# Performance work log

Measured on AMD Instinct MI355X. Metric: run time of the kernel, lower is better.

Reference implementation:

```python
import math
import jax, jax.numpy as jnp
import numpy as np

C = 256          # channels
HID = 64         # max(int(C*0.25),16)
RH = 64          # max(C//4,32) router hidden
N, S, H, W = 8, 64, 16, 16
LOW_FREQ_RATIO = 0.2
ROUTER_TEMP = 1.0
LN_EPS = 1e-5

def gelu(v):
    return jax.nn.gelu(v, approximate=False)

def bn1d(v, s, b):  # folded eval-mode BatchNorm1d: (N,C,S)
    return v * s[None, :, None] + b[None, :, None]

def conv1x1(v, w, b=None):  # v:(N,Cin,S), w:(Cout,Cin)
    o = jnp.einsum('oc,ncs->nos', w, v)
    if b is not None:
        o = o + b[None, :, None]
    return o

def convk(v, w):  # v:(N,Cin,S), w:(Cout,Cin,K), 'same' padding
    k = w.shape[-1]
    return jax.lax.conv_general_dilated(v, w, (1,), [(k // 2, k // 2)],
                                        dimension_numbers=('NCH', 'OIH', 'NCH'))

def setup_inputs():
    key = jax.random.key(0)
    ks = iter(jax.random.split(key, 64))
    def nrm(shape, sc=0.02):
        return jax.random.normal(next(ks), shape, jnp.float32) * sc
    d = {}
    d['x'] = jax.random.normal(next(ks), (N, C, S, H, W), jnp.float32)
    d['ln_g'] = jnp.ones((C,), jnp.float32)
    d['ln_b'] = jnp.zeros((C,), jnp.float32)
    for k in (3, 5, 7):
        d['mb_w%d' % k] = nrm((C, 3 * C, k))
        d['mb_s%d' % k] = 1.0 + nrm((C,))
        d['mb_b%d' % k] = nrm((C,))
    d['mf_w'] = nrm((C, C)); d['mf_s'] = 1.0 + nrm((C,)); d['mf_b'] = nrm((C,))
    d['pg_w1'] = nrm((HID, 3)); d['pg_s1'] = 1.0 + nrm((HID,)); d['pg_b1'] = nrm((HID,))
    d['pg_w2'] = nrm((C, HID)); d['pg_b2'] = nrm((C,))
    d['pp_w'] = nrm((C, C)); d['pp_s'] = 1.0 + nrm((C,)); d['pp_b'] = nrm((C,))
    d['mg_w'] = nrm((C, 2 * C)); d['mg_b'] = nrm((C,))
    d['mo_w1'] = nrm((C, 3 * C)); d['mo_s1'] = 1.0 + nrm((C,)); d['mo_b1'] = nrm((C,))
    d['mo_w2'] = nrm((C, C))
    d['rt_w1'] = nrm((RH, C + 5)); d['rt_b1'] = nrm((RH,))
    d['rt_w2'] = nrm((3, RH)); d['rt_b2'] = nrm((3,))
    d['bp_w1'] = nrm((C, 4 * C)); d['bp_s1'] = 1.0 + nrm((C,)); d['bp_b1'] = nrm((C,))
    d['bp_w2'] = nrm((C, C))
    d['res_scale'] = jnp.full((1, C, 1), 0.05, jnp.float32)
    d['fg_w'] = nrm((C, C)); d['fg_b'] = nrm((C,))
    d['sg_w'] = nrm((C, C)); d['sg_s'] = 1.0 + nrm((C,)); d['sg_b'] = nrm((C,))
    return d

def _forward(x, ln_g, ln_b, mb_w3, mb_s3, mb_b3, mb_w5, mb_s5, mb_b5,
             mb_w7, mb_s7, mb_b7, mf_w, mf_s, mf_b,
             pg_w1, pg_s1, pg_b1, pg_w2, pg_b2, pp_w, pp_s, pp_b,
             mg_w, mg_b, mo_w1, mo_s1, mo_b1, mo_w2,
             rt_w1, rt_b1, rt_w2, rt_b2, bp_w1, bp_s1, bp_b1, bp_w2,
             res_scale, fg_w, fg_b, sg_w, sg_s, sg_b):
    n, c, s = x.shape[:3]
    x32 = x.astype(jnp.float32)
    desc = x32.mean(axis=(-1, -2))                     # (N,C,S)
    t = desc.transpose(0, 2, 1)                        # (N,S,C)
    mu = t.mean(-1, keepdims=True)
    var = t.var(-1, keepdims=True)
    dn = (((t - mu) / jnp.sqrt(var + LN_EPS)) * ln_g + ln_b).transpose(0, 2, 1)  # (N,C,S)

    def tdiff(v, order):
        dd = v[:, :, order:] - v[:, :, :-order]
        return jnp.pad(dd, ((0, 0), (0, 0), (order, 0)))
    diff1 = tdiff(dn, 1)
    diff2 = tdiff(dn, 2)

    # motion branch (multi-kernel conv1d + BN + GELU)
    mi = jnp.concatenate([dn, diff1, diff2], axis=1)   # (N,3C,S)
    motion = 0.0
    for w, bs, bb in ((mb_w3, mb_s3, mb_b3), (mb_w5, mb_s5, mb_b5), (mb_w7, mb_s7, mb_b7)):
        motion = motion + gelu(bn1d(convk(mi, w), bs, bb))
    motion = gelu(bn1d(conv1x1(motion / 3.0, mf_w), mf_s, mf_b))

    # FFT-based cycle / phase estimation
    tokens = dn.transpose(0, 2, 1)                     # (N,S,C)
    freq = jnp.fft.rfft(tokens, axis=1, norm='ortho')  # (N,F,C) complex
    fe = jnp.abs(freq).mean(-1)                        # (N,F)
    Fb = fe.shape[1]
    low = min(max(int(round(Fb * LOW_FREQ_RATIO)), 1), Fb - 1)
    he = fe[:, low:]
    peak_rel = jnp.argmax(he, axis=-1)                 # (N,)
    peak_idx = peak_rel + low
    peak_val = jnp.take_along_axis(he, peak_rel[:, None], axis=1)
    cycle_conf = peak_val / jnp.maximum(he.sum(axis=1, keepdims=True), 1e-6)  # (N,1)
    peak_norm = peak_idx.astype(jnp.float32)[:, None] / float(Fb - 1)
    mean_freq = freq.mean(-1)                          # (N,F) complex
    dom = jnp.take_along_axis(mean_freq, peak_idx[:, None], axis=1)[:, 0]
    dom_phase = jnp.arctan2(dom.imag, dom.real)
    tax = jnp.arange(s, dtype=jnp.float32)
    ang = (2.0 * math.pi / max(s, 1)) * peak_idx.astype(jnp.float32)
    arg = ang[:, None] * tax[None, :] + dom_phase[:, None]
    phase_cos = jnp.cos(arg)[:, None, :]               # (N,1,S)
    phase_sin = jnp.sin(arg)[:, None, :]

    cycle_token = jnp.broadcast_to(cycle_conf[:, :, None], (n, 1, s))
    pf = jnp.concatenate([phase_cos, phase_sin, cycle_token], axis=1)  # (N,3,S)
    pgate = jax.nn.sigmoid(conv1x1(gelu(bn1d(conv1x1(pf, pg_w1), pg_s1, pg_b1)), pg_w2, pg_b2))
    phase = gelu(bn1d(conv1x1(dn * pgate, pp_w), pp_s, pp_b))

    # bidirectional EMA memory via lax.scan
    gate = jax.nn.sigmoid(conv1x1(jnp.concatenate([dn, jnp.abs(diff1)], axis=1), mg_w, mg_b))
    g = gate.transpose(2, 0, 1)                        # (S,N,C)
    dd = dn.transpose(2, 0, 1)
    def step(st, gd):
        gt, dt = gd
        st = gt * st + (1.0 - gt) * dt
        return st, st
    _, fo = jax.lax.scan(step, dd[0], (g[1:], dd[1:]))
    fwd_mem = jnp.concatenate([dd[:1], fo], axis=0).transpose(1, 2, 0)
    _, bo = jax.lax.scan(step, dd[-1], (g[-2::-1], dd[-2::-1]))
    bwd_mem = jnp.concatenate([dd[-1:], bo], axis=0)[::-1].transpose(1, 2, 0)
    memory = conv1x1(gelu(bn1d(conv1x1(
        jnp.concatenate([dn, fwd_mem, bwd_mem], axis=1), mo_w1), mo_s1, mo_b1)), mo_w2)

    # router
    seq_std = dn.std(axis=2).mean(axis=1, keepdims=True)
    diff_energy = jnp.abs(diff1).mean(axis=(1, 2))[:, None]
    motion_energy = jnp.abs(motion).mean(axis=(1, 2))[:, None]
    memory_energy = jnp.abs(memory - dn).mean(axis=(1, 2))[:, None]
    stats = jnp.concatenate([seq_std, diff_energy, cycle_conf, peak_norm,
                             memory_energy + motion_energy], axis=-1)
    ri = jnp.concatenate([dn.mean(-1), stats], axis=-1)  # (N,C+5)
    hdn = gelu(ri @ rt_w1.T + rt_b1)
    logits = hdn @ rt_w2.T + rt_b2
    bw = jax.nn.softmax(logits / max(ROUTER_TEMP, 1e-6), axis=-1)  # (N,3)
    fused = (bw[:, 0, None, None] * motion + bw[:, 1, None, None] * phase
             + bw[:, 2, None, None] * memory)

    delta = conv1x1(gelu(bn1d(conv1x1(
        jnp.concatenate([dn, fused, motion - phase, memory - dn], axis=1),
        bp_w1), bp_s1, bp_b1)), bp_w2)
    delta = delta * jax.nn.sigmoid(conv1x1(dn, fg_w, fg_b))
    delta = res_scale * delta
    delta = delta[:, :, :, None, None]                 # (N,C,S,1,1)

    sp = x32.mean(axis=2)                              # (N,C,H,W)
    sg_lin = jnp.einsum('oc,nchw->nohw', sg_w, sp)
    sgate = jax.nn.sigmoid(sg_lin * sg_s[None, :, None, None] + sg_b[None, :, None, None])
    delta = delta * sgate[:, :, None, :, :]            # (N,C,S,H,W)
    return x + delta.astype(x.dtype)

def reference(x, ln_g, ln_b, mb_w3, mb_s3, mb_b3, mb_w5, mb_s5, mb_b5,
              mb_w7, mb_s7, mb_b7, mf_w, mf_s, mf_b,
              pg_w1, pg_s1, pg_b1, pg_w2, pg_b2, pp_w, pp_s, pp_b,
              mg_w, mg_b, mo_w1, mo_s1, mo_b1, mo_w2,
              rt_w1, rt_b1, rt_w2, rt_b2, bp_w1, bp_s1, bp_b1, bp_w2,
              res_scale, fg_w, fg_b, sg_w, sg_s, sg_b):
    return _forward(x, ln_g, ln_b, mb_w3, mb_s3, mb_b3, mb_w5, mb_s5, mb_b5,
                    mb_w7, mb_s7, mb_b7, mf_w, mf_s, mf_b,
                    pg_w1, pg_s1, pg_b1, pg_w2, pg_b2, pp_w, pp_s, pp_b,
                    mg_w, mg_b, mo_w1, mo_s1, mo_b1, mo_w2,
                    rt_w1, rt_b1, rt_w2, rt_b2, bp_w1, bp_s1, bp_b1, bp_w2,
                    res_scale, fg_w, fg_b, sg_w, sg_s, sg_b)
```

## Files before the change

### kernel.cpp

```cpp
#include <hip/hip_runtime.h>
#include <math.h>

namespace {

constexpr int N_ = 8, C_ = 256, S_ = 64, HW_ = 256;
constexpr int NS = N_ * S_;
constexpr int NHW = N_ * HW_;

constexpr size_t O_DESC  = 0;
constexpr size_t O_DN    = 131072;
constexpr size_t O_MOT   = 393216;
constexpr size_t O_GATE  = 524288;
constexpr size_t O_MEM   = 786432;
constexpr size_t O_PHASE = 1048576;
constexpr size_t O_DELTA = 1441792;
constexpr size_t O_SCN   = 1572864;
constexpr size_t O_SPT   = 2752512;
constexpr size_t O_SGATE = 3276800;
constexpr size_t O_FE    = 3801088;
constexpr size_t O_MFRE  = 3801600;
constexpr size_t O_MFIM  = 3802112;
constexpr size_t O_BW    = 3802656;
constexpr size_t O_ATMF  = 3802688;
constexpr size_t O_ATMG  = 3868224;
constexpr size_t O_ATMO1 = 3999296;
constexpr size_t O_ATMO2 = 4195904;
constexpr size_t O_ATPP  = 4261440;
constexpr size_t O_ATBP1 = 4326976;
constexpr size_t O_ATBP2 = 4589120;
constexpr size_t O_ATFG  = 4654656;
constexpr size_t O_ATSG  = 4720192;
constexpr size_t O_WFRAG = 4785728;
constexpr size_t O_IM2   = 6850112;
constexpr size_t O_CONVC = 8226368;

typedef __attribute__((ext_vector_type(4))) float f32x4;
typedef __attribute__((ext_vector_type(8))) short s16x8;
typedef __attribute__((ext_vector_type(8))) unsigned short u16x8;

__device__ __forceinline__ float gelu_f(float v) {
  return 0.5f * v * (1.0f + erff(v * 0.70710678118654752f));
}
__device__ __forceinline__ float sigmoid_f(float v) {
  return 1.0f / (1.0f + expf(-v));
}
__device__ __forceinline__ unsigned short f2bf(float f) {
  unsigned int u = __float_as_uint(f);
  u += 0x7fffu + ((u >> 16) & 1u);
  return (unsigned short)(u >> 16);
}

__device__ __forceinline__ float block_sum256(float v, float* scratch) {
  #pragma unroll
  for (int off = 32; off; off >>= 1) v += __shfl_down(v, off, 64);
  int w = threadIdx.x >> 6;
  __syncthreads();
  if ((threadIdx.x & 63) == 0) scratch[w] = v;
  __syncthreads();
  return scratch[0] + scratch[1] + scratch[2] + scratch[3];
}

__device__ __forceinline__ void compute_pk(
    int n, const float* __restrict__ fe, const float* __restrict__ mfre,
    const float* __restrict__ mfim,
    float& conf, float& pnorm, float& dph, float& ang) {
  const float* f = fe + n * 33;
  float best = f[7]; int bidx = 0; float hs = 0.f;
  #pragma unroll
  for (int i = 0; i < 26; ++i) {
    float v = f[7 + i];
    hs += v;
    if (v > best) { best = v; bidx = i; }
  }
  int pi = bidx + 7;
  conf = best / fmaxf(hs, 1e-6f);
  pnorm = (float)pi * (1.f / 32.f);
  dph = atan2f(mfim[n * 33 + pi], mfre[n * 33 + pi]);
  ang = (6.283185307179586f / 64.f) * (float)pi;
}

__global__ __launch_bounds__(256) void weights_kernel(
    const float* __restrict__ wmf, const float* __restrict__ wmg,
    const float* __restrict__ wmo1, const float* __restrict__ wmo2,
    const float* __restrict__ wpp, const float* __restrict__ wbp1,
    const float* __restrict__ wbp2, const float* __restrict__ wfg,
    const float* __restrict__ wsg, float* __restrict__ ws,
    const float* __restrict__ w3, const float* __restrict__ w5,
    const float* __restrict__ w7, unsigned short* __restrict__ wf) {
  int bid = blockIdx.x;
  if (bid < 960) {
    __shared__ float tile[32][33];
    int xt = bid % 120, yt = bid / 120;
    const float* src; float* dst; int K;
    if      (xt < 8)   { src = wmf;  dst = ws + O_ATMF;  K = 256;  }
    else if (xt < 24)  { src = wmg;  dst = ws + O_ATMG;  K = 512;  xt -= 8;  }
    else if (xt < 48)  { src = wmo1; dst = ws + O_ATMO1; K = 768;  xt -= 24; }
    else if (xt < 56)  { src = wmo2; dst = ws + O_ATMO2; K = 256;  xt -= 48; }
    else if (xt < 64)  { src = wpp;  dst = ws + O_ATPP;  K = 256;  xt -= 56; }
    else if (xt < 96)  { src = wbp1; dst = ws + O_ATBP1; K = 1024; xt -= 64; }
    else if (xt < 104) { src = wbp2; dst = ws + O_ATBP2; K = 256;  xt -= 96; }
    else if (xt < 112) { src = wfg;  dst = ws + O_ATFG;  K = 256;  xt -= 104;}
    else               { src = wsg;  dst = ws + O_ATSG;  K = 256;  xt -= 112;}
    int tx = threadIdx.x & 31, ty = threadIdx.x >> 5;
    int c = xt * 32 + tx;
    #pragma unroll
    for (int i = 0; i < 4; ++i) {
      int r = yt * 32 + ty + i * 8;
      tile[ty + i * 8][tx] = src[(size_t)r * K + c];
    }
    __syncthreads();
    #pragma unroll
    for (int i = 0; i < 4; ++i) {
      int cc = xt * 32 + ty + i * 8;
      dst[(size_t)cc * 256 + yt * 32 + tx] = tile[tx][ty + i * 8];
    }
  } else {
    int g = (bid - 960) * 256 + threadIdx.x;
    int lane = g & 63;
    int m16 = (g >> 6) % 48;
    int kchunk = (g >> 6) / 48;
    int o = m16 * 16 + (lane & 15);
    int conv = o >> 8, oc = o & 255;
    int q = lane >> 4;
    u16x8 outv;
    #pragma unroll
    for (int j = 0; j < 8; ++j) {
      int k = kchunk * 32 + q * 8 + j;
      int ic = k / 7;
      int tau = k - ic * 7 - 3;
      float v = 0.f;
      if (conv == 0) {
        if (tau >= -1 && tau <= 1) v = w3[((size_t)oc * 768 + ic) * 3 + (tau + 1)];
      } else if (conv == 1) {
        if (tau >= -2 && tau <= 2) v = w5[((size_t)oc * 768 + ic) * 5 + (tau + 2)];
      } else {
        v = w7[((size_t)oc * 768 + ic) * 7 + (tau + 3)];
      }
      outv[j] = f2bf(v);
    }
    *((u16x8*)wf + g) = outv;
  }
}

__global__ __launch_bounds__(256) void reduce_x_kernel(
    const float* __restrict__ x, float* __restrict__ desc_t, float* __restrict__ sp_t) {
  int nc = blockIdx.x; int n = nc >> 8; int c = nc & 255;
  int t = threadIdx.x; int w = t >> 6; int l = t & 63;
  const float4* x4 = (const float4*)x + (size_t)nc * 4096;
  float4 sa = {0.f, 0.f, 0.f, 0.f};
  for (int i = 0; i < 16; ++i) {
    int s = w * 16 + i;
    float4 v = x4[(size_t)s * 64 + l];
    sa.x += v.x; sa.y += v.y; sa.z += v.z; sa.w += v.w;
    float ds = v.x + v.y + v.z + v.w;
    #pragma unroll
    for (int off = 32; off; off >>= 1) ds += __shfl_down(ds, off, 64);
    if (l == 0) desc_t[((size_t)n * 64 + s) * 256 + c] = ds * (1.f / 256.f);
  }
  __shared__ float4 lsp[4][64];
  lsp[w][l] = sa;
  __syncthreads();
  if (t < 64) {
    float4 a = lsp[0][t], b = lsp[1][t], c2 = lsp[2][t], d = lsp[3][t];
    float4 tot;
    tot.x = a.x + b.x + c2.x + d.x; tot.y = a.y + b.y + c2.y + d.y;
    tot.z = a.z + b.z + c2.z + d.z; tot.w = a.w + b.w + c2.w + d.w;
    size_t base = ((size_t)n * 256 + t * 4) * 256 + c;
    sp_t[base]       = tot.x * (1.f / 64.f);
    sp_t[base + 256] = tot.y * (1.f / 64.f);
    sp_t[base + 512] = tot.z * (1.f / 64.f);
    sp_t[base + 768] = tot.w * (1.f / 64.f);
  }
}

__global__ __launch_bounds__(256) void ln_kernel(
    const float* __restrict__ desc_t, const float* __restrict__ g,
    const float* __restrict__ b, float* __restrict__ dn_t) {
  __shared__ float sc[4];
  int col = blockIdx.x; int t = threadIdx.x;
  float v = desc_t[(size_t)col * 256 + t];
  float s1 = block_sum256(v, sc);
  float s2 = block_sum256(v * v, sc);
  float mu = s1 * (1.f / 256.f);
  float var = s2 * (1.f / 256.f) - mu * mu;
  float r = rsqrtf(var + 1e-5f);
  dn_t[(size_t)col * 256 + t] = (v - mu) * r * g[t] + b[t];
}

__global__ __launch_bounds__(256) void gate_kernel(
    const float* __restrict__ dn_t, const float* __restrict__ At_mg,
    const float* __restrict__ mg_b, float* __restrict__ gate_t) {
  __shared__ float gin[512];
  int col = blockIdx.x; int t = threadIdx.x; int s = col & 63;
  float d = dn_t[(size_t)col * 256 + t];
  float d1 = (s >= 1) ? d - dn_t[(size_t)(col - 1) * 256 + t] : 0.f;
  gin[t] = d;
  gin[256 + t] = fabsf(d1);
  __syncthreads();
  float a0 = 0.f, a1 = 0.f, a2 = 0.f, a3 = 0.f;
  #pragma unroll 4
  for (int k = 0; k < 512; k += 4) {
    a0 += At_mg[(size_t)(k + 0) * 256 + t] * gin[k + 0];
    a1 += At_mg[(size_t)(k + 1) * 256 + t] * gin[k + 1];
    a2 += At_mg[(size_t)(k + 2) * 256 + t] * gin[k + 2];
    a3 += At_mg[(size_t)(k + 3) * 256 + t] * gin[k + 3];
  }
  gate_t[(size_t)col * 256 + t] = sigmoid_f(((a0 + a1) + (a2 + a3)) + mg_b[t]);
}

__global__ __launch_bounds__(256) void dnaux_kernel(
    const float* __restrict__ dn_t, unsigned short* __restrict__ imf,
    float* __restrict__ fe, float* __restrict__ mfre, float* __restrict__ mfim) {
  int bid = blockIdx.x;
  int t = threadIdx.x;
  if (bid < 1344) {
    int g = bid * 256 + t;
    int lane = g & 63;
    int c16 = (g >> 6) % 32;
    int kchunk = (g >> 6) / 32;
    int col = c16 * 16 + (lane & 15);
    int n = col >> 6, s = col & 63;
    int q = lane >> 4;
    const float* base = dn_t + (size_t)n * 16384;
    u16x8 outv;
    #pragma unroll
    for (int j = 0; j < 8; ++j) {
      int k = kchunk * 32 + q * 8 + j;
      int ic = k / 7;
      int tau = k - ic * 7 - 3;
      int stream = ic >> 8, c = ic & 255;
      int sp = s + tau;
      float v = 0.f;
      if (sp >= 0 && sp < 64) {
        float d = base[(size_t)sp * 256 + c];
        if (stream == 0) v = d;
        else if (stream == 1) v = (sp >= 1) ? d - base[(size_t)(sp - 1) * 256 + c] : 0.f;
        else v = (sp >= 2) ? d - base[(size_t)(sp - 2) * 256 + c] : 0.f;
      }
      outv[j] = f2bf(v);
    }
    *((u16x8*)imf + g) = outv;
  } else {
    int b = bid - 1344; int n = b / 33; int f = b % 33;
    __shared__ float cs[64], sn[64];
    __shared__ float sc[4];
    if (t < 64) {
      int ft = (f * t) & 63;
      float ang = -6.283185307179586f * (float)ft * (1.f / 64.f);
      cs[t] = cosf(ang); sn[t] = sinf(ang);
    }
    __syncthreads();
    float re = 0.f, im = 0.f;
    const float* base = dn_t + (size_t)n * 16384 + t;
    for (int s = 0; s < 64; ++s) {
      float v = base[(size_t)s * 256];
      re += v * cs[s]; im += v * sn[s];
    }
    re *= 0.125f; im *= 0.125f;
    float mag = sqrtf(re * re + im * im);
    float sm = block_sum256(mag, sc);
    float sr = block_sum256(re, sc);
    float si = block_sum256(im, sc);
    if (t == 0) {
      fe[b]   = sm * (1.f / 256.f);
      mfre[b] = sr * (1.f / 256.f);
      mfim[b] = si * (1.f / 256.f);
    }
  }
}

__global__ __launch_bounds__(256) void conv_mfma_kernel(
    const unsigned short* __restrict__ wf, const unsigned short* __restrict__ imf,
    float* __restrict__ partial) {
  int mt = blockIdx.x, nt = blockIdx.y, kp = blockIdx.z;
  int lane = threadIdx.x & 63;
  int w = threadIdx.x >> 6;
  int m16 = mt * 4 + w;
  const s16x8* wfp = (const s16x8*)wf;
  const s16x8* imp = (const s16x8*)imf;
  f32x4 acc0 = {0.f,0.f,0.f,0.f}, acc1 = {0.f,0.f,0.f,0.f};
  f32x4 acc2 = {0.f,0.f,0.f,0.f}, acc3 = {0.f,0.f,0.f,0.f};
  #pragma unroll 2
  for (int cc = 0; cc < 42; ++cc) {
    int kc = kp * 42 + cc;
    s16x8 a = wfp[(size_t)(kc * 48 + m16) * 64 + lane];
    s16x8 b0 = imp[(size_t)(kc * 32 + nt * 4 + 0) * 64 + lane];
    s16x8 b1 = imp[(size_t)(kc * 32 + nt * 4 + 1) * 64 + lane];
    s16x8 b2 = imp[(size_t)(kc * 32 + nt * 4 + 2) * 64 + lane];
    s16x8 b3 = imp[(size_t)(kc * 32 + nt * 4 + 3) * 64 + lane];
    acc0 = __builtin_amdgcn_mfma_f32_16x16x32_bf16(a, b0, acc0, 0, 0, 0);
    acc1 = __builtin_amdgcn_mfma_f32_16x16x32_bf16(a, b1, acc1, 0, 0, 0);
    acc2 = __builtin_amdgcn_mfma_f32_16x16x32_bf16(a, b2, acc2, 0, 0, 0);
    acc3 = __builtin_amdgcn_mfma_f32_16x16x32_bf16(a, b3, acc3, 0, 0, 0);
  }
  int q = lane >> 4, ln = lane & 15;
  int o0 = m16 * 16 + q * 4;
  float* pb = partial + (size_t)kp * 393216;
  #pragma unroll
  for (int r = 0; r < 4; ++r) {
    size_t row = (size_t)(o0 + r) * 512;
    pb[row + (nt * 4 + 0) * 16 + ln] = acc0[r];
    pb[row + (nt * 4 + 1) * 16 + ln] = acc1[r];
    pb[row + (nt * 4 + 2) * 16 + ln] = acc2[r];
    pb[row + (nt * 4 + 3) * 16 + ln] = acc3[r];
  }
}

__global__ __launch_bounds__(256) void motion_kernel(
    const float* __restrict__ P,
    const float* __restrict__ s3, const float* __restrict__ b3,
    const float* __restrict__ s5, const float* __restrict__ b5,
    const float* __restrict__ s7, const float* __restrict__ b7,
    const float* __restrict__ At_mf, const float* __restrict__ mf_s,
    const float* __restrict__ mf_b, float* __restrict__ motion_t) {
  __shared__ float ms[256];
  int col = blockIdx.x; int t = threadIdx.x;
  float v3 = 0.f, v5 = 0.f, v7 = 0.f;
  #pragma unroll
  for (int kp = 0; kp < 4; ++kp) {
    size_t base = (size_t)kp * 393216 + col;
    v3 += P[base + (size_t)t * 512];
    v5 += P[base + (size_t)(t + 256) * 512];
    v7 += P[base + (size_t)(t + 512) * 512];
  }
  float tot = gelu_f(v3 * s3[t] + b3[t]) + gelu_f(v5 * s5[t] + b5[t]) + gelu_f(v7 * s7[t] + b7[t]);
  ms[t] = tot * (1.f / 3.f);
  __syncthreads();
  float a0 = 0.f, a1 = 0.f, a2 = 0.f, a3 = 0.f;
  #pragma unroll 4
  for (int k = 0; k < 256; k += 4) {
    a0 += At_mf[(size_t)(k + 0) * 256 + t] * ms[k + 0];
    a1 += At_mf[(size_t)(k + 1) * 256 + t] * ms[k + 1];
    a2 += At_mf[(size_t)(k + 2) * 256 + t] * ms[k + 2];
    a3 += At_mf[(size_t)(k + 3) * 256 + t] * ms[k + 3];
  }
  motion_t[(size_t)col * 256 + t] = gelu_f(((a0 + a1) + (a2 + a3)) * mf_s[t] + mf_b[t]);
}

__global__ __launch_bounds__(256) void scan_kernel(
    const float* __restrict__ dn_t, const float* __restrict__ gate_t, float* __restrict__ scn) {
  int n = blockIdx.x, half = blockIdx.y;
  int t = threadIdx.x;
  __shared__ float ld[64 * 128];
  __shared__ float lg[64 * 128];
  const float* dsrc = dn_t + (size_t)n * 16384 + half * 128;
  const float* gsrc = gate_t + (size_t)n * 16384 + half * 128;
  for (int i = t; i < 8192; i += 256) {
    int s = i >> 7, j = i & 127;
    ld[i] = dsrc[(size_t)s * 256 + j];
    lg[i] = gsrc[(size_t)s * 256 + j];
  }
  __syncthreads();
  int cl = t & 127;
  int c = half * 128 + cl;
  size_t ob = (size_t)n * 64 * 512 + c;
  if (t < 128) {
    float st = ld[cl];
    scn[ob] = st;
    for (int s = 1; s < 64; ++s) {
      float g = lg[s * 128 + cl], d = ld[s * 128 + cl];
      st = g * st + (1.f - g) * d;
      scn[ob + (size_t)s * 512] = st;
    }
  } else {
    float st = ld[63 * 128 + cl];
    scn[ob + (size_t)63 * 512 + 256] = st;
    for (int s = 62; s >= 0; --s) {
      float g = lg[s * 128 + cl], d = ld[s * 128 + cl];
      st = g * st + (1.f - g) * d;
      scn[ob + (size_t)s * 512 + 256] = st;
    }
  }
}

__global__ __launch_bounds__(256) void memory_kernel(
    const float* __restrict__ dn_t, const float* __restrict__ scn,
    const float* __restrict__ At1, const float* __restrict__ sc1, const float* __restrict__ bi1,
    const float* __restrict__ At2, float* __restrict__ mem_t) {
  __shared__ float bv[768];
  __shared__ float h[256];
  int col = blockIdx.x; int t = threadIdx.x;
  bv[t]       = dn_t[(size_t)col * 256 + t];
  bv[256 + t] = scn[(size_t)col * 512 + t];
  bv[512 + t] = scn[(size_t)col * 512 + 256 + t];
  __syncthreads();
  float a0 = 0.f, a1 = 0.f, a2 = 0.f, a3 = 0.f;
  #pragma unroll 4
  for (int k = 0; k < 768; k += 4) {
    a0 += At1[(size_t)(k + 0) * 256 + t] * bv[k + 0];
    a1 += At1[(size_t)(k + 1) * 256 + t] * bv[k + 1];
    a2 += At1[(size_t)(k + 2) * 256 + t] * bv[k + 2];
    a3 += At1[(size_t)(k + 3) * 256 + t] * bv[k + 3];
  }
  h[t] = gelu_f(((a0 + a1) + (a2 + a3)) * sc1[t] + bi1[t]);
  __syncthreads();
  float c0 = 0.f, c1 = 0.f, c2 = 0.f, c3 = 0.f;
  #pragma unroll 4
  for (int k = 0; k < 256; k += 4) {
    c0 += At2[(size_t)(k + 0) * 256 + t] * h[k + 0];
    c1 += At2[(size_t)(k + 1) * 256 + t] * h[k + 1];
    c2 += At2[(size_t)(k + 2) * 256 + t] * h[k + 2];
    c3 += At2[(size_t)(k + 3) * 256 + t] * h[k + 3];
  }
  mem_t[(size_t)col * 256 + t] = (c0 + c1) + (c2 + c3);
}

__global__ __launch_bounds__(256) void phase_kernel(
    const float* __restrict__ dn_t, const float* __restrict__ fe,
    const float* __restrict__ mfre, const float* __restrict__ mfim,
    const float* __restrict__ pg_w1, const float* __restrict__ pg_s1, const float* __restrict__ pg_b1,
    const float* __restrict__ pg_w2, const float* __restrict__ pg_b2,
    const float* __restrict__ At_pp, const float* __restrict__ pp_s, const float* __restrict__ pp_b,
    float* __restrict__ phase_t) {
  __shared__ float hh[64];
  __shared__ float pin[256];
  int col = blockIdx.x; int n = col >> 6; int s = col & 63; int t = threadIdx.x;
  float conf, pnorm, dph, ang;
  compute_pk(n, fe, mfre, mfim, conf, pnorm, dph, ang);
  (void)pnorm;
  float arg = ang * (float)s + dph;
  float pc = cosf(arg), ps = sinf(arg);
  if (t < 64) {
    float v = pg_w1[t * 3 + 0] * pc + pg_w1[t * 3 + 1] * ps + pg_w1[t * 3 + 2] * conf;
    hh[t] = gelu_f(v * pg_s1[t] + pg_b1[t]);
  }
  __syncthreads();
  float acc = pg_b2[t];
  const float* wrow = pg_w2 + t * 64;
  #pragma unroll 8
  for (int j = 0; j < 64; ++j) acc += wrow[j] * hh[j];
  pin[t] = dn_t[(size_t)col * 256 + t] * sigmoid_f(acc);
  __syncthreads();
  float a0 = 0.f, a1 = 0.f, a2 = 0.f, a3 = 0.f;
  #pragma unroll 4
  for (int k = 0; k < 256; k += 4) {
    a0 += At_pp[(size_t)(k + 0) * 256 + t] * pin[k + 0];
    a1 += At_pp[(size_t)(k + 1) * 256 + t] * pin[k + 1];
    a2 += At_pp[(size_t)(k + 2) * 256 + t] * pin[k + 2];
    a3 += At_pp[(size_t)(k + 3) * 256 + t] * pin[k + 3];
  }
  phase_t[(size_t)col * 256 + t] = gelu_f(((a0 + a1) + (a2 + a3)) * pp_s[t] + pp_b[t]);
}

__global__ __launch_bounds__(256) void router_kernel(
    const float* __restrict__ dn_t, const float* __restrict__ motion_t,
    const float* __restrict__ memory_t,
    const float* __restrict__ fe, const float* __restrict__ mfre,
    const float* __restrict__ mfim,
    const float* __restrict__ rt_w1, const float* __restrict__ rt_b1,
    const float* __restrict__ rt_w2, const float* __restrict__ rt_b2,
    float* __restrict__ bw) {
  int n = blockIdx.x; int c = threadIdx.x;
  __shared__ float ri[261];
  __shared__ float h2[64];
  __shared__ float lg[3];
  __shared__ float sc[4];
  float sum = 0.f, sq = 0.f, ad1 = 0.f, amot = 0.f, amem = 0.f, prev = 0.f;
  for (int s = 0; s < 64; ++s) {
    size_t i = ((size_t)n * 64 + s) * 256 + c;
    float d = dn_t[i];
    sum += d; sq += d * d;
    if (s > 0) ad1 += fabsf(d - prev);
    prev = d;
    amot += fabsf(motion_t[i]);
    amem += fabsf(memory_t[i] - d);
  }
  float mean = sum * (1.f / 64.f);
  float var = sq * (1.f / 64.f) - mean * mean;
  float stdc = sqrtf(fmaxf(var, 0.f));
  ri[c] = mean;
  float rstd = block_sum256(stdc, sc);
  float rad1 = block_sum256(ad1, sc);
  float rmot = block_sum256(amot, sc);
  float rmem = block_sum256(amem, sc);
  if (c == 0) {
    float conf, pnorm, dph, ang;
    compute_pk(n, fe, mfre, mfim, conf, pnorm, dph, ang);
    (void)dph; (void)ang;
    ri[256] = rstd * (1.f / 256.f);
    ri[257] = rad1 * (1.f / 16384.f);
    ri[258] = conf;
    ri[259] = pnorm;
    ri[260] = (rmem + rmot) * (1.f / 16384.f);
  }
  __syncthreads();
  if (c < 64) {
    float acc = rt_b1[c];
    const float* wrow = rt_w1 + c * 261;
    for (int i = 0; i < 261; ++i) acc += wrow[i] * ri[i];
    h2[c] = gelu_f(acc);
  }
  __syncthreads();
  if (c < 3) {
    float acc = rt_b2[c];
    const float* wrow = rt_w2 + c * 64;
    #pragma unroll 8
    for (int j = 0; j < 64; ++j) acc += wrow[j] * h2[j];
    lg[c] = acc;
  }
  __syncthreads();
  if (c == 0) {
    float m = fmaxf(lg[0], fmaxf(lg[1], lg[2]));
    float e0 = expf(lg[0] - m), e1 = expf(lg[1] - m), e2 = expf(lg[2] - m);
    float inv = 1.f / (e0 + e1 + e2);
    bw[n * 3 + 0] = e0 * inv; bw[n * 3 + 1] = e1 * inv; bw[n * 3 + 2] = e2 * inv;
  }
}

__global__ __launch_bounds__(256) void delta_kernel(
    const float* __restrict__ dn_t, const float* __restrict__ motion_t,
    const float* __restrict__ phase_t, const float* __restrict__ mem_t,
    const float* __restrict__ bw,
    const float* __restrict__ At_fg, const float* __restrict__ fg_b,
    const float* __restrict__ At1, const float* __restrict__ sc1, const float* __restrict__ bi1,
    const float* __restrict__ At2, const float* __restrict__ rs,
    float* __restrict__ delta_t) {
  __shared__ float bv[1024];
  __shared__ float h[256];
  int col = blockIdx.x; int n = col >> 6; int t = threadIdx.x;
  size_t i = (size_t)col * 256 + t;
  float d = dn_t[i], m = motion_t[i], p = phase_t[i], me = mem_t[i];
  float w0 = bw[n * 3 + 0], w1 = bw[n * 3 + 1], w2 = bw[n * 3 + 2];
  bv[t]       = d;
  bv[256 + t] = w0 * m + w1 * p + w2 * me;
  bv[512 + t] = m - p;
  bv[768 + t] = me - d;
  __syncthreads();
  float f0 = 0.f, f1 = 0.f, f2 = 0.f, f3 = 0.f;
  #pragma unroll 4
  for (int k = 0; k < 256; k += 4) {
    f0 += At_fg[(size_t)(k + 0) * 256 + t] * bv[k + 0];
    f1 += At_fg[(size_t)(k + 1) * 256 + t] * bv[k + 1];
    f2 += At_fg[(size_t)(k + 2) * 256 + t] * bv[k + 2];
    f3 += At_fg[(size_t)(k + 3) * 256 + t] * bv[k + 3];
  }
  float fgv = sigmoid_f(((f0 + f1) + (f2 + f3)) + fg_b[t]);
  float a0 = 0.f, a1 = 0.f, a2 = 0.f, a3 = 0.f;
  #pragma unroll 4
  for (int k = 0; k < 1024; k += 4) {
    a0 += At1[(size_t)(k + 0) * 256 + t] * bv[k + 0];
    a1 += At1[(size_t)(k + 1) * 256 + t] * bv[k + 1];
    a2 += At1[(size_t)(k + 2) * 256 + t] * bv[k + 2];
    a3 += At1[(size_t)(k + 3) * 256 + t] * bv[k + 3];
  }
  h[t] = gelu_f(((a0 + a1) + (a2 + a3)) * sc1[t] + bi1[t]);
  __syncthreads();
  float c0 = 0.f, c1 = 0.f, c2 = 0.f, c3 = 0.f;
  #pragma unroll 4
  for (int k = 0; k < 256; k += 4) {
    c0 += At2[(size_t)(k + 0) * 256 + t] * h[k + 0];
    c1 += At2[(size_t)(k + 1) * 256 + t] * h[k + 1];
    c2 += At2[(size_t)(k + 2) * 256 + t] * h[k + 2];
    c3 += At2[(size_t)(k + 3) * 256 + t] * h[k + 3];
  }
  delta_t[i] = ((c0 + c1) + (c2 + c3)) * fgv * rs[t];
}

template <int K, int EPI>
__global__ __launch_bounds__(256) void gemm_kernel(
    const float* __restrict__ At, const float* __restrict__ B, float* __restrict__ out,
    const float* __restrict__ sc, const float* __restrict__ bi,
    const float* __restrict__ fg, const float* __restrict__ rs) {
  int t = threadIdx.x;
  int o = blockIdx.x * 64 + (t & 63);
  int col = blockIdx.y * 4 + (t >> 6);
  const float* bp = B + (size_t)col * K;
  float4 a0 = {0.f,0.f,0.f,0.f};
  for (int kk = 0; kk < K; kk += 4) {
    float4 b0 = *(const float4*)(bp + kk);
    a0.x += At[(size_t)(kk + 0) * 256 + o] * b0.x;
    a0.y += At[(size_t)(kk + 1) * 256 + o] * b0.y;
    a0.z += At[(size_t)(kk + 2) * 256 + o] * b0.z;
    a0.w += At[(size_t)(kk + 3) * 256 + o] * b0.w;
  }
  float v0 = (a0.x + a0.y) + (a0.z + a0.w);
  if constexpr (EPI == 4) { v0 = sigmoid_f(v0 * sc[o] + bi[o]); }
  out[(size_t)col * 256 + o] = v0;
}

__global__ __launch_bounds__(256) void final_kernel(
    const float* __restrict__ x, const float* __restrict__ delta_t,
    const float* __restrict__ sgate_t, float* __restrict__ out) {
  int nc = blockIdx.x; int n = nc >> 8; int c = nc & 255;
  int t = threadIdx.x;
  __shared__ float dlt[64];
  __shared__ float4 sgs4[64];
  if (t < 64) dlt[t] = delta_t[((size_t)n * 64 + t) * 256 + c];
  ((float*)sgs4)[t] = sgate_t[((size_t)n * 256 + t) * 256 + c];
  __syncthreads();
  const float4* x4 = (const float4*)x + (size_t)nc * 4096;
  float4* o4 = (float4*)out + (size_t)nc * 4096;
  int w = t >> 6, l = t & 63;
  float4 sg = sgs4[l];
  for (int i = 0; i < 16; ++i) {
    int s = w * 16 + i;
    float d = dlt[s];
    float4 v = x4[(size_t)s * 64 + l];
    v.x += d * sg.x; v.y += d * sg.y; v.z += d * sg.z; v.w += d * sg.w;
    o4[(size_t)s * 64 + l] = v;
  }
}

}

extern "C" void kernel_launch(void* const* d_in, const int* in_sizes, int n_in,
                              void* d_out, int out_size, void* d_ws, size_t ws_size,
                              hipStream_t stream) {
  const float* x      = (const float*)d_in[0];
  const float* ln_g   = (const float*)d_in[1];
  const float* ln_b   = (const float*)d_in[2];
  const float* mb_w3  = (const float*)d_in[3];
  const float* mb_s3  = (const float*)d_in[4];
  const float* mb_b3  = (const float*)d_in[5];
  const float* mb_w5  = (const float*)d_in[6];
  const float* mb_s5  = (const float*)d_in[7];
  const float* mb_b5  = (const float*)d_in[8];
  const float* mb_w7  = (const float*)d_in[9];
  const float* mb_s7  = (const float*)d_in[10];
  const float* mb_b7  = (const float*)d_in[11];
  const float* mf_w   = (const float*)d_in[12];
  const float* mf_s   = (const float*)d_in[13];
  const float* mf_b   = (const float*)d_in[14];
  const float* pg_w1  = (const float*)d_in[15];
  const float* pg_s1  = (const float*)d_in[16];
  const float* pg_b1  = (const float*)d_in[17];
  const float* pg_w2  = (const float*)d_in[18];
  const float* pg_b2  = (const float*)d_in[19];
  const float* pp_w   = (const float*)d_in[20];
  const float* pp_s   = (const float*)d_in[21];
  const float* pp_b   = (const float*)d_in[22];
  const float* mg_w   = (const float*)d_in[23];
  const float* mg_b   = (const float*)d_in[24];
  const float* mo_w1  = (const float*)d_in[25];
  const float* mo_s1  = (const float*)d_in[26];
  const float* mo_b1  = (const float*)d_in[27];
  const float* mo_w2  = (const float*)d_in[28];
  const float* rt_w1  = (const float*)d_in[29];
  const float* rt_b1  = (const float*)d_in[30];
  const float* rt_w2  = (const float*)d_in[31];
  const float* rt_b2  = (const float*)d_in[32];
  const float* bp_w1  = (const float*)d_in[33];
  const float* bp_s1  = (const float*)d_in[34];
  const float* bp_b1  = (const float*)d_in[35];
  const float* bp_w2  = (const float*)d_in[36];
  const float* res_sc = (const float*)d_in[37];
  const float* fg_w   = (const float*)d_in[38];
  const float* fg_b   = (const float*)d_in[39];
  const float* sg_w   = (const float*)d_in[40];
  const float* sg_s   = (const float*)d_in[41];
  const float* sg_b   = (const float*)d_in[42];
  float* ws = (float*)d_ws;
  float* out = (float*)d_out;
  unsigned short* wfrag = (unsigned short*)(ws + O_WFRAG);
  unsigned short* im2   = (unsigned short*)(ws + O_IM2);

  weights_kernel<<<2976, 256, 0, stream>>>(mf_w, mg_w, mo_w1, mo_w2, pp_w, bp_w1,
      bp_w2, fg_w, sg_w, ws, mb_w3, mb_w5, mb_w7, wfrag);
  reduce_x_kernel<<<2048, 256, 0, stream>>>(x, ws + O_DESC, ws + O_SPT);
  ln_kernel<<<512, 256, 0, stream>>>(ws + O_DESC, ln_g, ln_b, ws + O_DN);
  gate_kernel<<<512, 256, 0, stream>>>(ws + O_DN, ws + O_ATMG, mg_b, ws + O_GATE);
  dnaux_kernel<<<1608, 256, 0, stream>>>(ws + O_DN, im2, ws + O_FE, ws + O_MFRE, ws + O_MFIM);
  conv_mfma_kernel<<<dim3(12, 8, 4), 256, 0, stream>>>(wfrag, im2, ws + O_CONVC);
  motion_kernel<<<512, 256, 0, stream>>>(ws + O_CONVC, mb_s3, mb_b3, mb_s5, mb_b5,
      mb_s7, mb_b7, ws + O_ATMF, mf_s, mf_b, ws + O_MOT);
  scan_kernel<<<dim3(8, 2), 256, 0, stream>>>(ws + O_DN, ws + O_GATE, ws + O_SCN);
  memory_kernel<<<512, 256, 0, stream>>>(ws + O_DN, ws + O_SCN, ws + O_ATMO1,
      mo_s1, mo_b1, ws + O_ATMO2, ws + O_MEM);
  phase_kernel<<<512, 256, 0, stream>>>(ws + O_DN, ws + O_FE, ws + O_MFRE, ws + O_MFIM,
      pg_w1, pg_s1, pg_b1, pg_w2, pg_b2, ws + O_ATPP, pp_s, pp_b, ws + O_PHASE);
  router_kernel<<<8, 256, 0, stream>>>(ws + O_DN, ws + O_MOT, ws + O_MEM,
      ws + O_FE, ws + O_MFRE, ws + O_MFIM, rt_w1, rt_b1, rt_w2, rt_b2, ws + O_BW);
  delta_kernel<<<512, 256, 0, stream>>>(ws + O_DN, ws + O_MOT, ws + O_PHASE, ws + O_MEM,
      ws + O_BW, ws + O_ATFG, fg_b, ws + O_ATBP1, bp_s1, bp_b1, ws + O_ATBP2, res_sc,
      ws + O_DELTA);
  gemm_kernel<256, 4><<<dim3(4, 512), 256, 0, stream>>>(ws + O_ATSG, ws + O_SPT,
      ws + O_SGATE, sg_s, sg_b, nullptr, nullptr);
  final_kernel<<<2048, 256, 0, stream>>>(x, ws + O_DELTA, ws + O_SGATE, out);
}
```

Measured before the change: 568.9 us.

## Merge independent stages into multi-role kernels and batch four columns per block

```diff
diff --git a/kernel.cpp b/kernel.cpp
--- a/kernel.cpp
+++ b/kernel.cpp
@@ -187,34 +187,46 @@
   dn_t[(size_t)col * 256 + t] = (v - mu) * r * g[t] + b[t];
 }
 
-__global__ __launch_bounds__(256) void gate_kernel(
+__global__ __launch_bounds__(256) void post_ln_kernel(
     const float* __restrict__ dn_t, const float* __restrict__ At_mg,
-    const float* __restrict__ mg_b, float* __restrict__ gate_t) {
-  __shared__ float gin[512];
-  int col = blockIdx.x; int t = threadIdx.x; int s = col & 63;
-  float d = dn_t[(size_t)col * 256 + t];
-  float d1 = (s >= 1) ? d - dn_t[(size_t)(col - 1) * 256 + t] : 0.f;
-  gin[t] = d;
-  gin[256 + t] = fabsf(d1);
-  __syncthreads();
-  float a0 = 0.f, a1 = 0.f, a2 = 0.f, a3 = 0.f;
-  #pragma unroll 4
-  for (int k = 0; k < 512; k += 4) {
-    a0 += At_mg[(size_t)(k + 0) * 256 + t] * gin[k + 0];
-    a1 += At_mg[(size_t)(k + 1) * 256 + t] * gin[k + 1];
-    a2 += At_mg[(size_t)(k + 2) * 256 + t] * gin[k + 2];
-    a3 += At_mg[(size_t)(k + 3) * 256 + t] * gin[k + 3];
-  }
-  gate_t[(size_t)col * 256 + t] = sigmoid_f(((a0 + a1) + (a2 + a3)) + mg_b[t]);
-}
-
-__global__ __launch_bounds__(256) void dnaux_kernel(
-    const float* __restrict__ dn_t, unsigned short* __restrict__ imf,
+    const float* __restrict__ mg_b, float* __restrict__ gate_t,
+    unsigned short* __restrict__ imf,
     float* __restrict__ fe, float* __restrict__ mfre, float* __restrict__ mfim) {
+  __shared__ __align__(16) float smem[2048];
   int bid = blockIdx.x;
   int t = threadIdx.x;
-  if (bid < 1344) {
-    int g = bid * 256 + t;
+  if (bid < 128) {
+    int c0 = bid * 4;
+    float4 f0, f1;
+    {
+      float d[4], a[4];
+      #pragma unroll
+      for (int i = 0; i < 4; ++i) {
+        int col = c0 + i; int s = col & 63;
+        float dd = dn_t[(size_t)col * 256 + t];
+        float d1 = (s >= 1) ? dd - dn_t[(size_t)(col - 1) * 256 + t] : 0.f;
+        d[i] = dd; a[i] = fabsf(d1);
+      }
+      f0.x = d[0]; f0.y = d[1]; f0.z = d[2]; f0.w = d[3];
+      f1.x = a[0]; f1.y = a[1]; f1.z = a[2]; f1.w = a[3];
+    }
+    *(float4*)&smem[t * 4] = f0;
+    *(float4*)&smem[(256 + t) * 4] = f1;
+    __syncthreads();
+    float a0 = 0.f, a1 = 0.f, a2 = 0.f, a3 = 0.f;
+    #pragma unroll 4
+    for (int k = 0; k < 512; ++k) {
+      float a = At_mg[(size_t)k * 256 + t];
+      float4 b = *(const float4*)&smem[k * 4];
+      a0 += a * b.x; a1 += a * b.y; a2 += a * b.z; a3 += a * b.w;
+    }
+    float bb = mg_b[t];
+    gate_t[(size_t)(c0 + 0) * 256 + t] = sigmoid_f(a0 + bb);
+    gate_t[(size_t)(c0 + 1) * 256 + t] = sigmoid_f(a1 + bb);
+    gate_t[(size_t)(c0 + 2) * 256 + t] = sigmoid_f(a2 + bb);
+    gate_t[(size_t)(c0 + 3) * 256 + t] = sigmoid_f(a3 + bb);
+  } else if (bid < 1472) {
+    int g = (bid - 128) * 256 + t;
     int lane = g & 63;
     int c16 = (g >> 6) % 32;
     int kchunk = (g >> 6) / 32;
@@ -241,9 +253,8 @@
     }
     *((u16x8*)imf + g) = outv;
   } else {
-    int b = bid - 1344; int n = b / 33; int f = b % 33;
-    __shared__ float cs[64], sn[64];
-    __shared__ float sc[4];
+    int b = bid - 1472; int n = b / 33; int f = b % 33;
+    float* cs = smem; float* sn = smem + 64; float* scr = smem + 128;
     if (t < 64) {
       int ft = (f * t) & 63;
       float ang = -6.283185307179586f * (float)ft * (1.f / 64.f);
@@ -258,9 +269,9 @@
     }
     re *= 0.125f; im *= 0.125f;
     float mag = sqrtf(re * re + im * im);
-    float sm = block_sum256(mag, sc);
-    float sr = block_sum256(re, sc);
-    float si = block_sum256(im, sc);
+    float sm = block_sum256(mag, scr);
+    float sr = block_sum256(re, scr);
+    float si = block_sum256(im, scr);
     if (t == 0) {
       fe[b]   = sm * (1.f / 256.f);
       mfre[b] = sr * (1.f / 256.f);
@@ -269,177 +280,252 @@
   }
 }
 
-__global__ __launch_bounds__(256) void conv_mfma_kernel(
+__global__ __launch_bounds__(256) void conv_scan_kernel(
     const unsigned short* __restrict__ wf, const unsigned short* __restrict__ imf,
-    float* __restrict__ partial) {
-  int mt = blockIdx.x, nt = blockIdx.y, kp = blockIdx.z;
-  int lane = threadIdx.x & 63;
-  int w = threadIdx.x >> 6;
-  int m16 = mt * 4 + w;
-  const s16x8* wfp = (const s16x8*)wf;
-  const s16x8* imp = (const s16x8*)imf;
-  f32x4 acc0 = {0.f,0.f,0.f,0.f}, acc1 = {0.f,0.f,0.f,0.f};
-  f32x4 acc2 = {0.f,0.f,0.f,0.f}, acc3 = {0.f,0.f,0.f,0.f};
-  #pragma unroll 2
-  for (int cc = 0; cc < 42; ++cc) {
-    int kc = kp * 42 + cc;
-    s16x8 a = wfp[(size_t)(kc * 48 + m16) * 64 + lane];
-    s16x8 b0 = imp[(size_t)(kc * 32 + nt * 4 + 0) * 64 + lane];
-    s16x8 b1 = imp[(size_t)(kc * 32 + nt * 4 + 1) * 64 + lane];
-    s16x8 b2 = imp[(size_t)(kc * 32 + nt * 4 + 2) * 64 + lane];
-    s16x8 b3 = imp[(size_t)(kc * 32 + nt * 4 + 3) * 64 + lane];
-    acc0 = __builtin_amdgcn_mfma_f32_16x16x32_bf16(a, b0, acc0, 0, 0, 0);
-    acc1 = __builtin_amdgcn_mfma_f32_16x16x32_bf16(a, b1, acc1, 0, 0, 0);
-    acc2 = __builtin_amdgcn_mfma_f32_16x16x32_bf16(a, b2, acc2, 0, 0, 0);
-    acc3 = __builtin_amdgcn_mfma_f32_16x16x32_bf16(a, b3, acc3, 0, 0, 0);
-  }
-  int q = lane >> 4, ln = lane & 15;
-  int o0 = m16 * 16 + q * 4;
-  float* pb = partial + (size_t)kp * 393216;
-  #pragma unroll
-  for (int r = 0; r < 4; ++r) {
-    size_t row = (size_t)(o0 + r) * 512;
-    pb[row + (nt * 4 + 0) * 16 + ln] = acc0[r];
-    pb[row + (nt * 4 + 1) * 16 + ln] = acc1[r];
-    pb[row + (nt * 4 + 2) * 16 + ln] = acc2[r];
-    pb[row + (nt * 4 + 3) * 16 + ln] = acc3[r];
-  }
-}
-
-__global__ __launch_bounds__(256) void motion_kernel(
+    float* __restrict__ partial,
+    const float* __restrict__ dn_t, const float* __restrict__ gate_t,
+    float* __restrict__ scn) {
+  __shared__ float smem[16384];
+  int bid = blockIdx.x;
+  int t = threadIdx.x;
+  if (bid < 384) {
+    int mt = bid % 12; int rem = bid / 12;
+    int nt = rem % 8; int kp = rem / 8;
+    int lane = t & 63;
+    int w = t >> 6;
+    int m16 = mt * 4 + w;
+    const s16x8* wfp = (const s16x8*)wf;
+    const s16x8* imp = (const s16x8*)imf;
+    f32x4 acc0 = {0.f,0.f,0.f,0.f}, acc1 = {0.f,0.f,0.f,0.f};
+    f32x4 acc2 = {0.f,0.f,0.f,0.f}, acc3 = {0.f,0.f,0.f,0.f};
+    #pragma unroll 2
+    for (int cc = 0; cc < 42; ++cc) {
+      int kc = kp * 42 + cc;
+      s16x8 a = wfp[(size_t)(kc * 48 + m16) * 64 + lane];
+      s16x8 b0 = imp[(size_t)(kc * 32 + nt * 4 + 0) * 64 + lane];
+      s16x8 b1 = imp[(size_t)(kc * 32 + nt * 4 + 1) * 64 + lane];
+      s16x8 b2 = imp[(size_t)(kc * 32 + nt * 4 + 2) * 64 + lane];
+      s16x8 b3 = imp[(size_t)(kc * 32 + nt * 4 + 3) * 64 + lane];
+      acc0 = __builtin_amdgcn_mfma_f32_16x16x32_bf16(a, b0, acc0, 0, 0, 0);
+      acc1 = __builtin_amdgcn_mfma_f32_16x16x32_bf16(a, b1, acc1, 0, 0, 0);
+      acc2 = __builtin_amdgcn_mfma_f32_16x16x32_bf16(a, b2, acc2, 0, 0, 0);
+      acc3 = __builtin_amdgcn_mfma_f32_16x16x32_bf16(a, b3, acc3, 0, 0, 0);
+    }
+    int q = lane >> 4, ln = lane & 15;
+    int o0 = m16 * 16 + q * 4;
+    float* pb = partial + (size_t)kp * 393216;
+    #pragma unroll
+    for (int r = 0; r < 4; ++r) {
+      size_t row = (size_t)(o0 + r) * 512;
+      pb[row + (nt * 4 + 0) * 16 + ln] = acc0[r];
+      pb[row + (nt * 4 + 1) * 16 + ln] = acc1[r];
+      pb[row + (nt * 4 + 2) * 16 + ln] = acc2[r];
+      pb[row + (nt * 4 + 3) * 16 + ln] = acc3[r];
+    }
+  } else {
+    int idx = bid - 384;
+    int n = idx >> 1, half = idx & 1;
+    float* ld = smem;
+    float* lg = smem + 8192;
+    const float* dsrc = dn_t + (size_t)n * 16384 + half * 128;
+    const float* gsrc = gate_t + (size_t)n * 16384 + half * 128;
+    for (int i = t; i < 8192; i += 256) {
+      int s = i >> 7, j = i & 127;
+      ld[i] = dsrc[(size_t)s * 256 + j];
+      lg[i] = gsrc[(size_t)s * 256 + j];
+    }
+    __syncthreads();
+    int cl = t & 127;
+    int c = half * 128 + cl;
+    size_t ob = (size_t)n * 64 * 512 + c;
+    if (t < 128) {
+      float st = ld[cl];
+      scn[ob] = st;
+      for (int s = 1; s < 64; ++s) {
+        float g = lg[s * 128 + cl], d = ld[s * 128 + cl];
+        st = g * st + (1.f - g) * d;
+        scn[ob + (size_t)s * 512] = st;
+      }
+    } else {
+      float st = ld[63 * 128 + cl];
+      scn[ob + (size_t)63 * 512 + 256] = st;
+      for (int s = 62; s >= 0; --s) {
+        float g = lg[s * 128 + cl], d = ld[s * 128 + cl];
+        st = g * st + (1.f - g) * d;
+        scn[ob + (size_t)s * 512 + 256] = st;
+      }
+    }
+  }
+}
+
+__global__ __launch_bounds__(256) void mid_kernel(
     const float* __restrict__ P,
     const float* __restrict__ s3, const float* __restrict__ b3,
     const float* __restrict__ s5, const float* __restrict__ b5,
     const float* __restrict__ s7, const float* __restrict__ b7,
     const float* __restrict__ At_mf, const float* __restrict__ mf_s,
-    const float* __restrict__ mf_b, float* __restrict__ motion_t) {
-  __shared__ float ms[256];
-  int col = blockIdx.x; int t = threadIdx.x;
-  float v3 = 0.f, v5 = 0.f, v7 = 0.f;
-  #pragma unroll
-  for (int kp = 0; kp < 4; ++kp) {
-    size_t base = (size_t)kp * 393216 + col;
-    v3 += P[base + (size_t)t * 512];
-    v5 += P[base + (size_t)(t + 256) * 512];
-    v7 += P[base + (size_t)(t + 512) * 512];
-  }
-  float tot = gelu_f(v3 * s3[t] + b3[t]) + gelu_f(v5 * s5[t] + b5[t]) + gelu_f(v7 * s7[t] + b7[t]);
-  ms[t] = tot * (1.f / 3.f);
-  __syncthreads();
-  float a0 = 0.f, a1 = 0.f, a2 = 0.f, a3 = 0.f;
-  #pragma unroll 4
-  for (int k = 0; k < 256; k += 4) {
-    a0 += At_mf[(size_t)(k + 0) * 256 + t] * ms[k + 0];
-    a1 += At_mf[(size_t)(k + 1) * 256 + t] * ms[k + 1];
-    a2 += At_mf[(size_t)(k + 2) * 256 + t] * ms[k + 2];
-    a3 += At_mf[(size_t)(k + 3) * 256 + t] * ms[k + 3];
-  }
-  motion_t[(size_t)col * 256 + t] = gelu_f(((a0 + a1) + (a2 + a3)) * mf_s[t] + mf_b[t]);
-}
-
-__global__ __launch_bounds__(256) void scan_kernel(
-    const float* __restrict__ dn_t, const float* __restrict__ gate_t, float* __restrict__ scn) {
-  int n = blockIdx.x, half = blockIdx.y;
-  int t = threadIdx.x;
-  __shared__ float ld[64 * 128];
-  __shared__ float lg[64 * 128];
-  const float* dsrc = dn_t + (size_t)n * 16384 + half * 128;
-  const float* gsrc = gate_t + (size_t)n * 16384 + half * 128;
-  for (int i = t; i < 8192; i += 256) {
-    int s = i >> 7, j = i & 127;
-    ld[i] = dsrc[(size_t)s * 256 + j];
-    lg[i] = gsrc[(size_t)s * 256 + j];
-  }
-  __syncthreads();
-  int cl = t & 127;
-  int c = half * 128 + cl;
-  size_t ob = (size_t)n * 64 * 512 + c;
-  if (t < 128) {
-    float st = ld[cl];
-    scn[ob] = st;
-    for (int s = 1; s < 64; ++s) {
-      float g = lg[s * 128 + cl], d = ld[s * 128 + cl];
-      st = g * st + (1.f - g) * d;
-      scn[ob + (size_t)s * 512] = st;
-    }
-  } else {
-    float st = ld[63 * 128 + cl];
-    scn[ob + (size_t)63 * 512 + 256] = st;
-    for (int s = 62; s >= 0; --s) {
-      float g = lg[s * 128 + cl], d = ld[s * 128 + cl];
-      st = g * st + (1.f - g) * d;
-      scn[ob + (size_t)s * 512 + 256] = st;
-    }
-  }
-}
-
-__global__ __launch_bounds__(256) void memory_kernel(
+    const float* __restrict__ mf_b, float* __restrict__ motion_t,
     const float* __restrict__ dn_t, const float* __restrict__ scn,
     const float* __restrict__ At1, const float* __restrict__ sc1, const float* __restrict__ bi1,
-    const float* __restrict__ At2, float* __restrict__ mem_t) {
-  __shared__ float bv[768];
-  __shared__ float h[256];
-  int col = blockIdx.x; int t = threadIdx.x;
-  bv[t]       = dn_t[(size_t)col * 256 + t];
-  bv[256 + t] = scn[(size_t)col * 512 + t];
-  bv[512 + t] = scn[(size_t)col * 512 + 256 + t];
-  __syncthreads();
-  float a0 = 0.f, a1 = 0.f, a2 = 0.f, a3 = 0.f;
-  #pragma unroll 4
-  for (int k = 0; k < 768; k += 4) {
-    a0 += At1[(size_t)(k + 0) * 256 + t] * bv[k + 0];
-    a1 += At1[(size_t)(k + 1) * 256 + t] * bv[k + 1];
-    a2 += At1[(size_t)(k + 2) * 256 + t] * bv[k + 2];
-    a3 += At1[(size_t)(k + 3) * 256 + t] * bv[k + 3];
-  }
-  h[t] = gelu_f(((a0 + a1) + (a2 + a3)) * sc1[t] + bi1[t]);
-  __syncthreads();
-  float c0 = 0.f, c1 = 0.f, c2 = 0.f, c3 = 0.f;
-  #pragma unroll 4
-  for (int k = 0; k < 256; k += 4) {
-    c0 += At2[(size_t)(k + 0) * 256 + t] * h[k + 0];
-    c1 += At2[(size_t)(k + 1) * 256 + t] * h[k + 1];
-    c2 += At2[(size_t)(k + 2) * 256 + t] * h[k + 2];
-    c3 += At2[(size_t)(k + 3) * 256 + t] * h[k + 3];
-  }
-  mem_t[(size_t)col * 256 + t] = (c0 + c1) + (c2 + c3);
-}
-
-__global__ __launch_bounds__(256) void phase_kernel(
-    const float* __restrict__ dn_t, const float* __restrict__ fe,
-    const float* __restrict__ mfre, const float* __restrict__ mfim,
+    const float* __restrict__ At2, float* __restrict__ mem_t,
+    const float* __restrict__ fe, const float* __restrict__ mfre, const float* __restrict__ mfim,
     const float* __restrict__ pg_w1, const float* __restrict__ pg_s1, const float* __restrict__ pg_b1,
     const float* __restrict__ pg_w2, const float* __restrict__ pg_b2,
     const float* __restrict__ At_pp, const float* __restrict__ pp_s, const float* __restrict__ pp_b,
-    float* __restrict__ phase_t) {
-  __shared__ float hh[64];
-  __shared__ float pin[256];
-  int col = blockIdx.x; int n = col >> 6; int s = col & 63; int t = threadIdx.x;
-  float conf, pnorm, dph, ang;
-  compute_pk(n, fe, mfre, mfim, conf, pnorm, dph, ang);
-  (void)pnorm;
-  float arg = ang * (float)s + dph;
-  float pc = cosf(arg), ps = sinf(arg);
-  if (t < 64) {
-    float v = pg_w1[t * 3 + 0] * pc + pg_w1[t * 3 + 1] * ps + pg_w1[t * 3 + 2] * conf;
-    hh[t] = gelu_f(v * pg_s1[t] + pg_b1[t]);
-  }
-  __syncthreads();
-  float acc = pg_b2[t];
-  const float* wrow = pg_w2 + t * 64;
-  #pragma unroll 8
-  for (int j = 0; j < 64; ++j) acc += wrow[j] * hh[j];
-  pin[t] = dn_t[(size_t)col * 256 + t] * sigmoid_f(acc);
-  __syncthreads();
-  float a0 = 0.f, a1 = 0.f, a2 = 0.f, a3 = 0.f;
-  #pragma unroll 4
-  for (int k = 0; k < 256; k += 4) {
-    a0 += At_pp[(size_t)(k + 0) * 256 + t] * pin[k + 0];
-    a1 += At_pp[(size_t)(k + 1) * 256 + t] * pin[k + 1];
-    a2 += At_pp[(size_t)(k + 2) * 256 + t] * pin[k + 2];
-    a3 += At_pp[(size_t)(k + 3) * 256 + t] * pin[k + 3];
-  }
-  phase_t[(size_t)col * 256 + t] = gelu_f(((a0 + a1) + (a2 + a3)) * pp_s[t] + pp_b[t]);
+    float* __restrict__ phase_t,
+    const float* __restrict__ At_sg, const float* __restrict__ sp_t,
+    const float* __restrict__ sg_s, const float* __restrict__ sg_b,
+    float* __restrict__ sgate_t) {
+  __shared__ __align__(16) float smem[4096];
+  int bid = blockIdx.x;
+  int t = threadIdx.x;
+  if (bid < 128) {
+    int c0 = bid * 4;
+    float4 v3 = {0,0,0,0}, v5 = {0,0,0,0}, v7 = {0,0,0,0};
+    #pragma unroll
+    for (int kp = 0; kp < 4; ++kp) {
+      const float* base = P + (size_t)kp * 393216 + c0;
+      float4 x3 = *(const float4*)(base + (size_t)t * 512);
+      float4 x5 = *(const float4*)(base + (size_t)(t + 256) * 512);
+      float4 x7 = *(const float4*)(base + (size_t)(t + 512) * 512);
+      v3.x += x3.x; v3.y += x3.y; v3.z += x3.z; v3.w += x3.w;
+      v5.x += x5.x; v5.y += x5.y; v5.z += x5.z; v5.w += x5.w;
+      v7.x += x7.x; v7.y += x7.y; v7.z += x7.z; v7.w += x7.w;
+    }
+    float s3v = s3[t], b3v = b3[t], s5v = s5[t], b5v = b5[t], s7v = s7[t], b7v = b7[t];
+    float4 ms;
+    ms.x = (gelu_f(v3.x*s3v+b3v) + gelu_f(v5.x*s5v+b5v) + gelu_f(v7.x*s7v+b7v)) * (1.f/3.f);
+    ms.y = (gelu_f(v3.y*s3v+b3v) + gelu_f(v5.y*s5v+b5v) + gelu_f(v7.y*s7v+b7v)) * (1.f/3.f);
+    ms.z = (gelu_f(v3.z*s3v+b3v) + gelu_f(v5.z*s5v+b5v) + gelu_f(v7.z*s7v+b7v)) * (1.f/3.f);
+    ms.w = (gelu_f(v3.w*s3v+b3v) + gelu_f(v5.w*s5v+b5v) + gelu_f(v7.w*s7v+b7v)) * (1.f/3.f);
+    *(float4*)&smem[t * 4] = ms;
+    __syncthreads();
+    float a0 = 0.f, a1 = 0.f, a2 = 0.f, a3 = 0.f;
+    #pragma unroll 4
+    for (int k = 0; k < 256; ++k) {
+      float a = At_mf[(size_t)k * 256 + t];
+      float4 b = *(const float4*)&smem[k * 4];
+      a0 += a * b.x; a1 += a * b.y; a2 += a * b.z; a3 += a * b.w;
+    }
+    float sv = mf_s[t], bv2 = mf_b[t];
+    motion_t[(size_t)(c0 + 0) * 256 + t] = gelu_f(a0 * sv + bv2);
+    motion_t[(size_t)(c0 + 1) * 256 + t] = gelu_f(a1 * sv + bv2);
+    motion_t[(size_t)(c0 + 2) * 256 + t] = gelu_f(a2 * sv + bv2);
+    motion_t[(size_t)(c0 + 3) * 256 + t] = gelu_f(a3 * sv + bv2);
+  } else if (bid < 256) {
+    int c0 = (bid - 128) * 4;
+    float* bv = smem;
+    float* h4 = smem + 3072;
+    float4 r0, r1, r2;
+    #pragma unroll
+    for (int i = 0; i < 4; ++i) {
+      int col = c0 + i;
+      ((float*)&r0)[i] = dn_t[(size_t)col * 256 + t];
+      ((float*)&r1)[i] = scn[(size_t)col * 512 + t];
+      ((float*)&r2)[i] = scn[(size_t)col * 512 + 256 + t];
+    }
+    *(float4*)&bv[t * 4] = r0;
+    *(float4*)&bv[(256 + t) * 4] = r1;
+    *(float4*)&bv[(512 + t) * 4] = r2;
+    __syncthreads();
+    float a0 = 0.f, a1 = 0.f, a2 = 0.f, a3 = 0.f;
+    #pragma unroll 4
+    for (int k = 0; k < 768; ++k) {
+      float a = At1[(size_t)k * 256 + t];
+      float4 b = *(const float4*)&bv[k * 4];
+      a0 += a * b.x; a1 += a * b.y; a2 += a * b.z; a3 += a * b.w;
+    }
+    float sv = sc1[t], bb = bi1[t];
+    float4 h;
+    h.x = gelu_f(a0 * sv + bb); h.y = gelu_f(a1 * sv + bb);
+    h.z = gelu_f(a2 * sv + bb); h.w = gelu_f(a3 * sv + bb);
+    *(float4*)&h4[t * 4] = h;
+    __syncthreads();
+    float c0a = 0.f, c1a = 0.f, c2a = 0.f, c3a = 0.f;
+    #pragma unroll 4
+    for (int k = 0; k < 256; ++k) {
+      float a = At2[(size_t)k * 256 + t];
+      float4 b = *(const float4*)&h4[k * 4];
+      c0a += a * b.x; c1a += a * b.y; c2a += a * b.z; c3a += a * b.w;
+    }
+    mem_t[(size_t)(c0 + 0) * 256 + t] = c0a;
+    mem_t[(size_t)(c0 + 1) * 256 + t] = c1a;
+    mem_t[(size_t)(c0 + 2) * 256 + t] = c2a;
+    mem_t[(size_t)(c0 + 3) * 256 + t] = c3a;
+  } else if (bid < 384) {
+    int c0 = (bid - 256) * 4; int n = c0 >> 6; int s0 = c0 & 63;
+    float* hh4 = smem;
+    float* pin4 = smem + 256;
+    float conf, pnorm, dph, ang;
+    compute_pk(n, fe, mfre, mfim, conf, pnorm, dph, ang);
+    (void)pnorm;
+    if (t < 64) {
+      float w0 = pg_w1[t * 3 + 0], w1 = pg_w1[t * 3 + 1], w2 = pg_w1[t * 3 + 2];
+      float sv = pg_s1[t], bb = pg_b1[t];
+      float4 hv;
+      #pragma unroll
+      for (int i = 0; i < 4; ++i) {
+        float arg = ang * (float)(s0 + i) + dph;
+        float v = w0 * cosf(arg) + w1 * sinf(arg) + w2 * conf;
+        ((float*)&hv)[i] = gelu_f(v * sv + bb);
+      }
+      *(float4*)&hh4[t * 4] = hv;
+    }
+    __syncthreads();
+    float p0, p1, p2, p3;
+    {
+      float bb = pg_b2[t];
+      float a0 = bb, a1 = bb, a2 = bb, a3 = bb;
+      const float* wrow = pg_w2 + t * 64;
+      #pragma unroll 8
+      for (int j = 0; j < 64; ++j) {
+        float w = wrow[j];
+        float4 h = *(const float4*)&hh4[j * 4];
+        a0 += w * h.x; a1 += w * h.y; a2 += w * h.z; a3 += w * h.w;
+      }
+      p0 = sigmoid_f(a0); p1 = sigmoid_f(a1); p2 = sigmoid_f(a2); p3 = sigmoid_f(a3);
+    }
+    float4 pin;
+    pin.x = dn_t[(size_t)(c0 + 0) * 256 + t] * p0;
+    pin.y = dn_t[(size_t)(c0 + 1) * 256 + t] * p1;
+    pin.z = dn_t[(size_t)(c0 + 2) * 256 + t] * p2;
+    pin.w = dn_t[(size_t)(c0 + 3) * 256 + t] * p3;
+    *(float4*)&pin4[t * 4] = pin;
+    __syncthreads();
+    float a0 = 0.f, a1 = 0.f, a2 = 0.f, a3 = 0.f;
+    #pragma unroll 4
+    for (int k = 0; k < 256; ++k) {
+      float a = At_pp[(size_t)k * 256 + t];
+      float4 b = *(const float4*)&pin4[k * 4];
+      a0 += a * b.x; a1 += a * b.y; a2 += a * b.z; a3 += a * b.w;
+    }
+    float sv = pp_s[t], bb = pp_b[t];
+    phase_t[(size_t)(c0 + 0) * 256 + t] = gelu_f(a0 * sv + bb);
+    phase_t[(size_t)(c0 + 1) * 256 + t] = gelu_f(a1 * sv + bb);
+    phase_t[(size_t)(c0 + 2) * 256 + t] = gelu_f(a2 * sv + bb);
+    phase_t[(size_t)(c0 + 3) * 256 + t] = gelu_f(a3 * sv + bb);
+  } else {
+    int c0 = (bid - 384) * 4;
+    float4 r0;
+    #pragma unroll
+    for (int i = 0; i < 4; ++i) {
+      ((float*)&r0)[i] = sp_t[(size_t)(c0 + i) * 256 + t];
+    }
+    *(float4*)&smem[t * 4] = r0;
+    __syncthreads();
+    float a0 = 0.f, a1 = 0.f, a2 = 0.f, a3 = 0.f;
+    #pragma unroll 4
+    for (int k = 0; k < 256; ++k) {
+      float a = At_sg[(size_t)k * 256 + t];
+      float4 b = *(const float4*)&smem[k * 4];
+      a0 += a * b.x; a1 += a * b.y; a2 += a * b.z; a3 += a * b.w;
+    }
+    float sv = sg_s[t], bb = sg_b[t];
+    sgate_t[(size_t)(c0 + 0) * 256 + t] = sigmoid_f(a0 * sv + bb);
+    sgate_t[(size_t)(c0 + 1) * 256 + t] = sigmoid_f(a1 * sv + bb);
+    sgate_t[(size_t)(c0 + 2) * 256 + t] = sigmoid_f(a2 * sv + bb);
+    sgate_t[(size_t)(c0 + 3) * 256 + t] = sigmoid_f(a3 * sv + bb);
+  }
 }
 
 __global__ __launch_bounds__(256) void router_kernel(
@@ -515,67 +601,67 @@
     const float* __restrict__ At1, const float* __restrict__ sc1, const float* __restrict__ bi1,
     const float* __restrict__ At2, const float* __restrict__ rs,
     float* __restrict__ delta_t) {
-  __shared__ float bv[1024];
-  __shared__ float h[256];
-  int col = blockIdx.x; int n = col >> 6; int t = threadIdx.x;
-  size_t i = (size_t)col * 256 + t;
-  float d = dn_t[i], m = motion_t[i], p = phase_t[i], me = mem_t[i];
+  __shared__ __align__(16) float smem[5120];
+  float* bv = smem;
+  float* h4 = smem + 4096;
+  int bid = blockIdx.x;
+  int c0 = bid * 4; int n = c0 >> 6; int t = threadIdx.x;
   float w0 = bw[n * 3 + 0], w1 = bw[n * 3 + 1], w2 = bw[n * 3 + 2];
-  bv[t]       = d;
-  bv[256 + t] = w0 * m + w1 * p + w2 * me;
-  bv[512 + t] = m - p;
-  bv[768 + t] = me - d;
-  __syncthreads();
-  float f0 = 0.f, f1 = 0.f, f2 = 0.f, f3 = 0.f;
-  #pragma unroll 4
-  for (int k = 0; k < 256; k += 4) {
-    f0 += At_fg[(size_t)(k + 0) * 256 + t] * bv[k + 0];
-    f1 += At_fg[(size_t)(k + 1) * 256 + t] * bv[k + 1];
-    f2 += At_fg[(size_t)(k + 2) * 256 + t] * bv[k + 2];
-    f3 += At_fg[(size_t)(k + 3) * 256 + t] * bv[k + 3];
-  }
-  float fgv = sigmoid_f(((f0 + f1) + (f2 + f3)) + fg_b[t]);
+  float4 fd, ffu, fmp, fmd;
+  #pragma unroll
+  for (int i = 0; i < 4; ++i) {
+    size_t idx = (size_t)(c0 + i) * 256 + t;
+    float d = dn_t[idx], m = motion_t[idx], p = phase_t[idx], me = mem_t[idx];
+    ((float*)&fd)[i] = d;
+    ((float*)&ffu)[i] = w0 * m + w1 * p + w2 * me;
+    ((float*)&fmp)[i] = m - p;
+    ((float*)&fmd)[i] = me - d;
+  }
+  *(float4*)&bv[t * 4] = fd;
+  *(float4*)&bv[(256 + t) * 4] = ffu;
+  *(float4*)&bv[(512 + t) * 4] = fmp;
+  *(float4*)&bv[(768 + t) * 4] = fmd;
+  __syncthreads();
+  float fg0, fg1, fg2, fg3;
+  {
+    float a0 = 0.f, a1 = 0.f, a2 = 0.f, a3 = 0.f;
+    #pragma unroll 4
+    for (int k = 0; k < 256; ++k) {
+      float a = At_fg[(size_t)k * 256 + t];
+      float4 b = *(const float4*)&bv[k * 4];
+      a0 += a * b.x; a1 += a * b.y; a2 += a * b.z; a3 += a * b.w;
+    }
+    float bb = fg_b[t];
+    fg0 = sigmoid_f(a0 + bb); fg1 = sigmoid_f(a1 + bb);
+    fg2 = sigmoid_f(a2 + bb); fg3 = sigmoid_f(a3 + bb);
+  }
+  {
+    float a0 = 0.f, a1 = 0.f, a2 = 0.f, a3 = 0.f;
+    #pragma unroll 4
+    for (int k = 0; k < 1024; ++k) {
+      float a = At1[(size_t)k * 256 + t];
+      float4 b = *(const float4*)&bv[k * 4];
+      a0 += a * b.x; a1 += a * b.y; a2 += a * b.z; a3 += a * b.w;
+    }
+    float sv = sc1[t], bb = bi1[t];
+    float4 h;
+    h.x = gelu_f(a0 * sv + bb); h.y = gelu_f(a1 * sv + bb);
+    h.z = gelu_f(a2 * sv + bb); h.w = gelu_f(a3 * sv + bb);
+    *(float4*)&h4[t * 4] = h;
+  }
+  __syncthreads();
   float a0 = 0.f, a1 = 0.f, a2 = 0.f, a3 = 0.f;
   #pragma unroll 4
-  for (int k = 0; k < 1024; k += 4) {
-    a0 += At1[(size_t)(k + 0) * 256 + t] * bv[k + 0];
-    a1 += At1[(size_t)(k + 1) * 256 + t] * bv[k + 1];
-    a2 += At1[(size_t)(k + 2) * 256 + t] * bv[k + 2];
-    a3 += At1[(size_t)(k + 3) * 256 + t] * bv[k + 3];
-  }
-  h[t] = gelu_f(((a0 + a1) + (a2 + a3)) * sc1[t] + bi1[t]);
-  __syncthreads();
-  float c0 = 0.f, c1 = 0.f, c2 = 0.f, c3 = 0.f;
-  #pragma unroll 4
-  for (int k = 0; k < 256; k += 4) {
-    c0 += At2[(size_t)(k + 0) * 256 + t] * h[k + 0];
-    c1 += At2[(size_t)(k + 1) * 256 + t] * h[k + 1];
-    c2 += At2[(size_t)(k + 2) * 256 + t] * h[k + 2];
-    c3 += At2[(size_t)(k + 3) * 256 + t] * h[k + 3];
-  }
-  delta_t[i] = ((c0 + c1) + (c2 + c3)) * fgv * rs[t];
-}
-
-template <int K, int EPI>
-__global__ __launch_bounds__(256) void gemm_kernel(
-    const float* __restrict__ At, const float* __restrict__ B, float* __restrict__ out,
-    const float* __restrict__ sc, const float* __restrict__ bi,
-    const float* __restrict__ fg, const float* __restrict__ rs) {
-  int t = threadIdx.x;
-  int o = blockIdx.x * 64 + (t & 63);
-  int col = blockIdx.y * 4 + (t >> 6);
-  const float* bp = B + (size_t)col * K;
-  float4 a0 = {0.f,0.f,0.f,0.f};
-  for (int kk = 0; kk < K; kk += 4) {
-    float4 b0 = *(const float4*)(bp + kk);
-    a0.x += At[(size_t)(kk + 0) * 256 + o] * b0.x;
-    a0.y += At[(size_t)(kk + 1) * 256 + o] * b0.y;
-    a0.z += At[(size_t)(kk + 2) * 256 + o] * b0.z;
-    a0.w += At[(size_t)(kk + 3) * 256 + o] * b0.w;
-  }
-  float v0 = (a0.x + a0.y) + (a0.z + a0.w);
-  if constexpr (EPI == 4) { v0 = sigmoid_f(v0 * sc[o] + bi[o]); }
-  out[(size_t)col * 256 + o] = v0;
+  for (int k = 0; k < 256; ++k) {
+    float a = At2[(size_t)k * 256 + t];
+    float4 b = *(const float4*)&h4[k * 4];
+    a0 += a * b.x; a1 += a * b.y; a2 += a * b.z; a3 += a * b.w;
+  }
+  float rsv = rs[t];
+  delta_t[(size_t)(c0 + 0) * 256 + t] = a0 * fg0 * rsv;
+  delta_t[(size_t)(c0 + 1) * 256 + t] = a1 * fg1 * rsv;
+  delta_t[(size_t)(c0 + 2) * 256 + t] = a2 * fg2 * rsv;
+  delta_t[(size_t)(c0 + 3) * 256 + t] = a3 * fg3 * rsv;
 }
 
 __global__ __launch_bounds__(256) void final_kernel(
@@ -658,22 +744,20 @@
       bp_w2, fg_w, sg_w, ws, mb_w3, mb_w5, mb_w7, wfrag);
   reduce_x_kernel<<<2048, 256, 0, stream>>>(x, ws + O_DESC, ws + O_SPT);
   ln_kernel<<<512, 256, 0, stream>>>(ws + O_DESC, ln_g, ln_b, ws + O_DN);
-  gate_kernel<<<512, 256, 0, stream>>>(ws + O_DN, ws + O_ATMG, mg_b, ws + O_GATE);
-  dnaux_kernel<<<1608, 256, 0, stream>>>(ws + O_DN, im2, ws + O_FE, ws + O_MFRE, ws + O_MFIM);
-  conv_mfma_kernel<<<dim3(12, 8, 4), 256, 0, stream>>>(wfrag, im2, ws + O_CONVC);
-  motion_kernel<<<512, 256, 0, stream>>>(ws + O_CONVC, mb_s3, mb_b3, mb_s5, mb_b5,
-      mb_s7, mb_b7, ws + O_ATMF, mf_s, mf_b, ws + O_MOT);
-  scan_kernel<<<dim3(8, 2), 256, 0, stream>>>(ws + O_DN, ws + O_GATE, ws + O_SCN);
-  memory_kernel<<<512, 256, 0, stream>>>(ws + O_DN, ws + O_SCN, ws + O_ATMO1,
-      mo_s1, mo_b1, ws + O_ATMO2, ws + O_MEM);
-  phase_kernel<<<512, 256, 0, stream>>>(ws + O_DN, ws + O_FE, ws + O_MFRE, ws + O_MFIM,
-      pg_w1, pg_s1, pg_b1, pg_w2, pg_b2, ws + O_ATPP, pp_s, pp_b, ws + O_PHASE);
+  post_ln_kernel<<<1736, 256, 0, stream>>>(ws + O_DN, ws + O_ATMG, mg_b, ws + O_GATE,
+      im2, ws + O_FE, ws + O_MFRE, ws + O_MFIM);
+  conv_scan_kernel<<<400, 256, 0, stream>>>(wfrag, im2, ws + O_CONVC,
+      ws + O_DN, ws + O_GATE, ws + O_SCN);
+  mid_kernel<<<896, 256, 0, stream>>>(ws + O_CONVC, mb_s3, mb_b3, mb_s5, mb_b5,
+      mb_s7, mb_b7, ws + O_ATMF, mf_s, mf_b, ws + O_MOT,
+      ws + O_DN, ws + O_SCN, ws + O_ATMO1, mo_s1, mo_b1, ws + O_ATMO2, ws + O_MEM,
+      ws + O_FE, ws + O_MFRE, ws + O_MFIM,
+      pg_w1, pg_s1, pg_b1, pg_w2, pg_b2, ws + O_ATPP, pp_s, pp_b, ws + O_PHASE,
+      ws + O_ATSG, ws + O_SPT, sg_s, sg_b, ws + O_SGATE);
   router_kernel<<<8, 256, 0, stream>>>(ws + O_DN, ws + O_MOT, ws + O_MEM,
       ws + O_FE, ws + O_MFRE, ws + O_MFIM, rt_w1, rt_b1, rt_w2, rt_b2, ws + O_BW);
-  delta_kernel<<<512, 256, 0, stream>>>(ws + O_DN, ws + O_MOT, ws + O_PHASE, ws + O_MEM,
+  delta_kernel<<<128, 256, 0, stream>>>(ws + O_DN, ws + O_MOT, ws + O_PHASE, ws + O_MEM,
       ws + O_BW, ws + O_ATFG, fg_b, ws + O_ATBP1, bp_s1, bp_b1, ws + O_ATBP2, res_sc,
       ws + O_DELTA);
-  gemm_kernel<256, 4><<<dim3(4, 512), 256, 0, stream>>>(ws + O_ATSG, ws + O_SPT,
-      ws + O_SGATE, sg_s, sg_b, nullptr, nullptr);
   final_kernel<<<2048, 256, 0, stream>>>(x, ws + O_DELTA, ws + O_SGATE, out);
 }
```

New measurement: 638.2 us. 12.2% more time.
